# Performance work log

Measured on AMD Instinct MI355X. Metric: run time of the kernel, lower is better.

## Reference

```python
import jax, jax.numpy as jnp
import numpy as np

N_USER, N_ITEM, N_ENT, N_REL, D = 100000, 50000, 200000, 32, 64
N_EDGE, NNZ = 500000, 2000000
N_HOPS, N_GCN, RES_LAMBDA = 2, 2, 0.5
MIN_NORM = 1e-15
BALL_EPS = 1e-3  # Poincare ball (c=1) boundary clip, standard fp32 value


def _sqnorm(x):
    return jnp.sum(x * x, axis=-1, keepdims=True)


def _norm(x):
    return jnp.maximum(jnp.sqrt(_sqnorm(x)), MIN_NORM)


def project(x):
    # clip points to the open unit ball
    n = _norm(x)
    maxn = 1.0 - BALL_EPS
    return jnp.where(n > maxn, x / n * maxn, x)


def expmap0(u):
    # exp map at origin, c=1: tanh(||u||) * u/||u||
    n = _norm(u)
    return jnp.tanh(n) * u / n


def mobius_add(x, y):
    x2, y2 = _sqnorm(x), _sqnorm(y)
    xy = jnp.sum(x * y, axis=-1, keepdims=True)
    num = (1.0 + 2.0 * xy + y2) * x + (1.0 - x2) * y
    den = 1.0 + 2.0 * xy + x2 * y2
    return num / jnp.maximum(den, MIN_NORM)


def expmap(u, p):
    # exp map at base point p of tangent vector u
    n = _norm(u)
    lam = 2.0 / jnp.maximum(1.0 - _sqnorm(p), MIN_NORM)
    return mobius_add(p, jnp.tanh(0.5 * lam * n) * u / n)


def logmap(x, p):
    # log map at base point p of point x
    sub = mobius_add(-p, x)
    n = _norm(sub)
    lam = 2.0 / jnp.maximum(1.0 - _sqnorm(p), MIN_NORM)
    return (2.0 / lam) * jnp.arctanh(jnp.minimum(n, 1.0 - 1e-5)) * sub / n


def l2norm(x):
    # F.normalize(x, dim=-1), eps=1e-12
    return x / jnp.maximum(jnp.linalg.norm(x, axis=-1, keepdims=True), 1e-12)


def rgat_agg(ent, rel, head, tail, rtype):
    he, te, re = ent[head], ent[tail], rel[rtype]  # [E, D] gathers
    ricci = l2norm(te + re)
    hh = expmap0(he)
    ht = expmap(te, hh)
    hr = expmap(re, hh)
    res = project(mobius_add(ht, hr))
    res = logmap(res, hh) + ricci * 1e-7
    res = jax.nn.relu(res)
    sums = jax.ops.segment_sum(res, head, num_segments=N_ENT)
    cnt = jax.ops.segment_sum(jnp.ones((head.shape[0], 1), res.dtype), head, num_segments=N_ENT)
    return sums / jnp.maximum(cnt, 1.0)  # scatter_mean


def setup_inputs() -> dict:
    key = jax.random.key(0)
    ks = jax.random.split(key, 9)
    return {
        "uEmbeds": jax.random.normal(ks[0], (N_USER, D), jnp.float32) * 0.02,
        "eEmbeds": jax.random.normal(ks[1], (N_ENT, D), jnp.float32) * 0.02,
        "rEmbeds": jax.random.normal(ks[2], (N_REL, D), jnp.float32) * 0.02,
        "adj_val": jax.random.uniform(ks[8], (NNZ,), jnp.float32),
        "edge_head": jax.random.randint(ks[3], (N_EDGE,), 0, N_ENT),
        "edge_tail": jax.random.randint(ks[4], (N_EDGE,), 0, N_ENT),
        "edge_type": jax.random.randint(ks[5], (N_EDGE,), 1, N_REL),
        "adj_row": jax.random.randint(ks[6], (NNZ,), 0, N_USER + N_ITEM),
        "adj_col": jax.random.randint(ks[7], (NNZ,), 0, N_USER + N_ITEM),
    }


def reference(uEmbeds, eEmbeds, rEmbeds, adj_val, edge_head, edge_tail, edge_type, adj_row, adj_col):
    rtype = edge_type - 1
    ent_res = eEmbeds
    ent = eEmbeds
    for _ in range(N_HOPS):  # RGAT hops (mess_dropout=False for determinism)
        ent = rgat_agg(ent, rEmbeds, edge_head, edge_tail, rtype)
        ent = l2norm(ent)
        ent_res = RES_LAMBDA * ent_res + ent
    # concat users with first n_items entity embeddings
    embeds = jnp.concatenate([uEmbeds, ent_res[:N_ITEM]], axis=0)  # [user+item, D]
    total = embeds
    cur = embeds
    for _ in range(N_GCN):  # GCN layers: spmm(adj, embeds) in COO form
        cur = jax.ops.segment_sum(adj_val[:, None] * cur[adj_col], adj_row,
                                  num_segments=N_USER + N_ITEM)
        total = total + cur
    # original returns (total[:N_USER], total[N_USER:]); we return the concat
    return total
```

## Files before the change

kernel.cpp:

```cpp
#include <hip/hip_runtime.h>
#include <math.h>

#define D 64
#define MIN_NORM 1e-15f
#define NBINS 64
#define MAXBKT 1024
#define L1_TILE 4096

#define RCP(x)  __builtin_amdgcn_rcpf(x)
#define RSQ(x)  __builtin_amdgcn_rsqf(x)

template <int CTRL>
__device__ __forceinline__ float dpp_sum_step(float v) {
    int iv = __builtin_bit_cast(int, v);
    int sh = __builtin_amdgcn_update_dpp(0, iv, CTRL, 0xf, 0xf, true);
    return v + __builtin_bit_cast(float, sh);
}
#define DPP_XOR1  0xB1
#define DPP_XOR2  0x4E
#define DPP_HMIR  0x141
#define DPP_MIR   0x140

__device__ __forceinline__ float row16_sum(float v) {
    v = dpp_sum_step<DPP_XOR1>(v);
    v = dpp_sum_step<DPP_XOR2>(v);
    v = dpp_sum_step<DPP_HMIR>(v);
    v = dpp_sum_step<DPP_MIR>(v);
    return v;
}


__device__ __forceinline__ float fast_tanh_pos(float x) {
    float t = __expf(-2.0f * x);
    return (1.0f - t) * RCP(1.0f + t);
}

__device__ __forceinline__ float fast_atanh(float x) {
    return 0.5f * __logf((1.0f + x) * RCP(1.0f - x));
}


__global__ void rel_prep_kernel(const float* __restrict__ rel,
                                float* __restrict__ rtab, int n_rel)
{
    int r = threadIdx.x;
    if (r >= n_rel) return;
    float s = 0.0f;
    for (int d = 0; d < D; ++d) { float v = rel[r * D + d]; s += v * v; }
    float re2g = fmaxf(s, 1e-30f);
    float rn  = RSQ(re2g);
    float nre = re2g * rn;
    float a   = fast_tanh_pos(1.0f);
    float rm2 = RCP(fmaxf(1.0f - a * a, MIN_NORM));
    rtab[r]       = s;
    rtab[64 + r]  = rn;
    rtab[128 + r] = nre;
    rtab[192 + r] = fast_tanh_pos(nre * rm2) * rn;
}


template <int HOP>
__global__ __launch_bounds__(256) void rgat_head_kernel(
    const float* __restrict__ ent, const float* __restrict__ rel,
    const int* __restrict__ erow_ptr, const int2* __restrict__ pair_e,
    const int* __restrict__ headperm,
    const float* __restrict__ prev_res,
    const float* __restrict__ rtab, float* __restrict__ te2tab,
    float* __restrict__ ent_out, float* __restrict__ res_out,
    int n_ent)
{
    int g = blockIdx.x * 16 + (threadIdx.x >> 4);
    if (g >= n_ent) return;
    int sub = threadIdx.x & 15;
    int h = headperm[g];

    const float* hp = ent + (size_t)h * D + sub;
    float hex = hp[0], hey = hp[16], hez = hp[32], hew = hp[48];

    float HE2, a, HH2, mterm, rmterm, bconst;
    if (HOP == 1) {
        HE2 = row16_sum(hex*hex + hey*hey + hez*hez + hew*hew);
        float HE2g = fmaxf(HE2, 1e-30f);
        float rNhe = RSQ(HE2g);
        float Nhe  = HE2g * rNhe;
        a = fast_tanh_pos(Nhe) * rNhe;
        HH2 = a * a * HE2;
        mterm = fmaxf(1.0f - HH2, MIN_NORM);
        rmterm = RCP(mterm);
        bconst = 0.0f;
    } else {
        HE2 = 1.0f;
        a = fast_tanh_pos(1.0f);
        HH2 = a * a;
        mterm = 1.0f - HH2;
        rmterm = RCP(mterm);
        bconst = fast_tanh_pos(rmterm);
    }

    float ax = 0.0f, ay = 0.0f, az = 0.0f, aw = 0.0f;
    int s = erow_ptr[h];
    int e = erow_ptr[h + 1];

    for (int i = s; i < e; ++i) {
        int2 pe = pair_e[i];
        int tcol = pe.x;
        int rr = pe.y - 1;
        const float* tp = ent + (size_t)tcol * D + sub;
        const float* rp = rel + (size_t)rr * D + sub;
        float tex = tp[0], tey = tp[16], tez = tp[32], tew = tp[48];
        float rex = rp[0], rey = rp[16], rez = rp[32], rew = rp[48];

        float HT = row16_sum(hex*tex + hey*tey + hez*tez + hew*tew);
        float HR = row16_sum(hex*rex + hey*rey + hez*rez + hew*rew);
        float TR = row16_sum(tex*rex + tey*rey + tez*rez + tew*rew);

        float TE2;
        if (HOP == 1) TE2 = row16_sum(tex*tex + tey*tey + tez*tez + tew*tew);
        else          TE2 = te2tab[tcol];

        float RE2  = rtab[rr];
        float rNre = rtab[64 + rr];

        float ricci_k = 1e-7f * RSQ(fmaxf(TE2 + 2.0f * TR + RE2, 1e-24f));

        float b, c;
        if (HOP == 1) {
            float TE2g = fmaxf(TE2, 1e-30f);
            float rNte = RSQ(TE2g);
            b = fast_tanh_pos(TE2g * rNte * rmterm) * rNte;
            c = fast_tanh_pos(rtab[128 + rr] * rmterm) * rNre;
        } else {
            b = bconst;
            c = rtab[192 + rr];
        }

        float y2t = b * b * TE2, xyt = a * b * HT;
        float A1 = 1.0f + 2.0f * xyt + y2t, B1 = 1.0f - HH2;
        float r_d1 = RCP(fmaxf(1.0f + 2.0f * xyt + HH2 * y2t, MIN_NORM));
        float p1 = A1 * a * r_d1, q1 = B1 * b * r_d1;
        float HT2 = fmaxf((A1*A1*HH2 + 2.0f*A1*B1*xyt + B1*B1*y2t) * r_d1 * r_d1, 0.0f);

        float y2r = c * c * RE2, xyr = a * c * HR;
        float A2 = 1.0f + 2.0f * xyr + y2r, B2 = 1.0f - HH2;
        float r_d2 = RCP(fmaxf(1.0f + 2.0f * xyr + HH2 * y2r, MIN_NORM));
        float p2 = A2 * a * r_d2, q2 = B2 * c * r_d2;
        float HR2 = fmaxf((A2*A2*HH2 + 2.0f*A2*B2*xyr + B2*B2*y2r) * r_d2 * r_d2, 0.0f);

        float xy3 = p1*p2*HE2 + p1*q2*HR + q1*p2*HT + q1*q2*TR;
        float A3 = 1.0f + 2.0f * xy3 + HR2, B3 = 1.0f - HT2;
        float r_d3 = RCP(fmaxf(1.0f + 2.0f * xy3 + HT2 * HR2, MIN_NORM));
        float al = (A3 * p1 + B3 * p2) * r_d3;
        float be = A3 * q1 * r_d3;
        float ga = B3 * q2 * r_d3;
        float R2 = fmaxf((A3*A3*HT2 + 2.0f*A3*B3*xy3 + B3*B3*HR2) * r_d3 * r_d3, 0.0f);

        float R2g = fmaxf(R2, 1e-30f);
        float rNr = RSQ(R2g);
        float Nr  = R2g * rNr;
        const float maxn = 1.0f - 1e-3f;
        if (Nr > maxn) {
            float sc = maxn * rNr;
            al *= sc; be *= sc; ga *= sc;
            R2 = maxn * maxn;
        }

        float dhr = a * (al * HE2 + be * HT + ga * HR);
        float xy4 = -dhr;
        float A4 = 1.0f + 2.0f * xy4 + R2, B4 = 1.0f - HH2;
        float r_d4 = RCP(fmaxf(1.0f + 2.0f * xy4 + HH2 * R2, MIN_NORM));
        float sh = (-A4 * a + B4 * al) * r_d4;
        float st = B4 * be * r_d4;
        float sr = B4 * ga * r_d4;
        float SUB2 = fmaxf((A4*A4*HH2 + 2.0f*A4*B4*xy4 + B4*B4*R2) * r_d4 * r_d4, 0.0f);

        float SUB2g = fmaxf(SUB2, 1e-30f);
        float rNsub = RSQ(SUB2g);
        float Nsub  = SUB2g * rNsub;
        float k = mterm * fast_atanh(fminf(Nsub, 1.0f - 1e-5f)) * rNsub;

        float kh = k * sh;
        float kt = k * st + ricci_k;
        float kr = k * sr + ricci_k;

        ax += fmaxf(kh*hex + kt*tex + kr*rex, 0.0f);
        ay += fmaxf(kh*hey + kt*tey + kr*rey, 0.0f);
        az += fmaxf(kh*hez + kt*tez + kr*rez, 0.0f);
        aw += fmaxf(kh*hew + kt*tew + kr*rew, 0.0f);
    }

    float rc = RCP(fmaxf((float)(e - s), 1.0f));
    float mx = ax*rc, my = ay*rc, mz = az*rc, mw = aw*rc;
    float M2 = row16_sum(mx*mx + my*my + mz*mz + mw*mw);
    float rn = RSQ(fmaxf(M2, 1e-24f));
    mx *= rn; my *= rn; mz *= rn; mw *= rn;

    if (HOP == 1) {
        float* ep = ent_out + (size_t)h * D + sub;
        ep[0] = mx; ep[16] = my; ep[32] = mz; ep[48] = mw;
        if (sub == 0) te2tab[h] = (M2 > 1e-24f) ? 1.0f : 0.0f;
    }
    const float* pp = prev_res + (size_t)h * D + sub;
    float* rp2 = res_out + (size_t)h * D + sub;
    rp2[0]  = 0.5f*pp[0]  + mx;
    rp2[16] = 0.5f*pp[16] + my;
    rp2[32] = 0.5f*pp[32] + mz;
    rp2[48] = 0.5f*pp[48] + mw;
}


__global__ __launch_bounds__(256) void deg_hist_kernel(
    const int* __restrict__ erow_ptr, int* __restrict__ dbins, int n_heads)
{
    __shared__ int lbin[NBINS];
    int tid = threadIdx.x;
    if (tid < NBINS) lbin[tid] = 0;
    __syncthreads();
    int h = blockIdx.x * 256 + tid;
    if (h < n_heads) {
        int d = min(erow_ptr[h + 1] - erow_ptr[h], NBINS - 1);
        atomicAdd(&lbin[d], 1);
    }
    __syncthreads();
    if (tid < NBINS) { int c = lbin[tid]; if (c) atomicAdd(&dbins[tid], c); }
}

__global__ void deg_scan_kernel(const int* __restrict__ dbins, int* __restrict__ bin_cursor)
{
    int tid = threadIdx.x;
    int v = dbins[tid];
    int incl = v;
#pragma unroll
    for (int off = 1; off < 64; off <<= 1) {
        int u = __shfl_up(incl, off, 64);
        if (tid >= off) incl += u;
    }
    int T = __shfl(incl, 63, 64);
    bin_cursor[tid] = T - incl;
}

__global__ __launch_bounds__(256) void deg_scatter_kernel(
    const int* __restrict__ erow_ptr, int* __restrict__ bin_cursor,
    int* __restrict__ headperm, int n_heads)
{
    __shared__ int lbin[NBINS];
    __shared__ int lbase[NBINS];
    int tid = threadIdx.x;
    if (tid < NBINS) lbin[tid] = 0;
    __syncthreads();
    int h = blockIdx.x * 256 + tid;
    int b = 0, lpos = 0;
    bool act = (h < n_heads);
    if (act) {
        b = min(erow_ptr[h + 1] - erow_ptr[h], NBINS - 1);
        lpos = atomicAdd(&lbin[b], 1);
    }
    __syncthreads();
    if (tid < NBINS) { int c = lbin[tid]; lbase[tid] = c ? atomicAdd(&bin_cursor[tid], c) : 0; }
    __syncthreads();
    if (act) headperm[lbase[b] + lpos] = h;
}


__global__ void concat_init_kernel(const float4* __restrict__ u,
                                   const float4* __restrict__ res,
                                   float4* __restrict__ bufA,
                                   int user4, int total4)
{
    int i = blockIdx.x * blockDim.x + threadIdx.x;
    if (i >= total4) return;
    float4 v = (i < user4) ? u[i] : res[i - user4];
    bufA[i] = v;
}


__global__ void hist_kernel(const int* __restrict__ row, int* __restrict__ counts, int nnz)
{
    int i = blockIdx.x * blockDim.x + threadIdx.x;
    if (i < nnz) atomicAdd(&counts[row[i]], 1);
}

__global__ __launch_bounds__(256) void block_scan_kernel(
    const int* __restrict__ counts, int* __restrict__ local_scan,
    int* __restrict__ block_sums, int n)
{
    __shared__ int wsum[4];
    int tid  = threadIdx.x;
    int lane = tid & 63;
    int wave = tid >> 6;
    int base = blockIdx.x * 1024 + tid * 4;

    int4 v = make_int4(0, 0, 0, 0);
    if (base + 3 < n) {
        v = *(const int4*)(counts + base);
    } else {
        if (base + 0 < n) v.x = counts[base + 0];
        if (base + 1 < n) v.y = counts[base + 1];
        if (base + 2 < n) v.z = counts[base + 2];
        if (base + 3 < n) v.w = counts[base + 3];
    }
    int total = v.x + v.y + v.z + v.w;

    int incl = total;
#pragma unroll
    for (int off = 1; off < 64; off <<= 1) {
        int u = __shfl_up(incl, off, 64);
        if (lane >= off) incl += u;
    }
    if (lane == 63) wsum[wave] = incl;
    __syncthreads();
    int woff = 0;
    for (int w = 0; w < wave; ++w) woff += wsum[w];
    int excl = woff + incl - total;

    if (tid == 255) block_sums[blockIdx.x] = woff + incl;

    int p0 = excl;
    int p1 = p0 + v.x;
    int p2 = p1 + v.y;
    int p3 = p2 + v.z;
    if (base + 3 < n) {
        *(int4*)(local_scan + base) = make_int4(p0, p1, p2, p3);
    } else {
        if (base + 0 < n) local_scan[base + 0] = p0;
        if (base + 1 < n) local_scan[base + 1] = p1;
        if (base + 2 < n) local_scan[base + 2] = p2;
        if (base + 3 < n) local_scan[base + 3] = p3;
    }
}

__global__ __launch_bounds__(256) void scan_blocksums_kernel(
    const int* __restrict__ block_sums, int* __restrict__ block_offs,
    int* __restrict__ row_ptr, int n, int nb)
{
    __shared__ int lds[256];
    int tid = threadIdx.x;
    int v = (tid < nb) ? block_sums[tid] : 0;
    lds[tid] = v;
    __syncthreads();
    for (int off = 1; off < 256; off <<= 1) {
        int t = (tid >= off) ? lds[tid - off] : 0;
        __syncthreads();
        lds[tid] += t;
        __syncthreads();
    }
    block_offs[tid] = lds[tid] - v;
    if (tid == nb - 1) row_ptr[n] = lds[tid];
}

__global__ void apply_offsets_kernel(const int* __restrict__ local_scan,
                                     const int* __restrict__ block_offs,
                                     int* __restrict__ row_ptr,
                                     int* __restrict__ cursor,
                                     int* __restrict__ bktcur, int n)
{
    int i = blockIdx.x * blockDim.x + threadIdx.x;
    if (i >= n) return;
    int v = local_scan[i] + block_offs[i >> 10];
    row_ptr[i] = v;
    cursor[i]  = v;
    if ((i & 255) == 0) bktcur[i >> 8] = v;
}


__global__ __launch_bounds__(256) void bucket_l1_kernel(
    const int* __restrict__ key, const int* __restrict__ col,
    const int* __restrict__ vbits,
    int* __restrict__ bktcur, int2* __restrict__ bkt,
    int n, int nbkt)
{
    __shared__ int lcnt[MAXBKT];
    __shared__ int lofs[MAXBKT];
    __shared__ int gofs[MAXBKT];
    __shared__ int lpos[MAXBKT];
    __shared__ int wsum[4];
    __shared__ int2 lent[L1_TILE];
    __shared__ unsigned short lbkt[L1_TILE];

    int tid  = threadIdx.x;
    int lane = tid & 63;
    int wave = tid >> 6;
    int base = blockIdx.x * L1_TILE;
    int cnt_total = min(n - base, L1_TILE);

    for (int b = tid; b < MAXBKT; b += 256) lcnt[b] = 0;
    __syncthreads();

#pragma unroll
    for (int k = 0; k < L1_TILE / 256; ++k) {
        int i = base + k * 256 + tid;
        if (i < n) atomicAdd(&lcnt[key[i] >> 8], 1);
    }
    __syncthreads();

    int b0 = tid * 4;
    int c0 = lcnt[b0], c1 = lcnt[b0 + 1], c2 = lcnt[b0 + 2], c3 = lcnt[b0 + 3];
    int tot = c0 + c1 + c2 + c3;
    int incl = tot;
#pragma unroll
    for (int off = 1; off < 64; off <<= 1) {
        int u = __shfl_up(incl, off, 64);
        if (lane >= off) incl += u;
    }
    if (lane == 63) wsum[wave] = incl;
    __syncthreads();
    int woff = 0;
    for (int w = 0; w < wave; ++w) woff += wsum[w];
    int excl = woff + incl - tot;
    lofs[b0]     = excl;                lpos[b0]     = excl;
    lofs[b0 + 1] = excl + c0;           lpos[b0 + 1] = excl + c0;
    lofs[b0 + 2] = excl + c0 + c1;      lpos[b0 + 2] = excl + c0 + c1;
    lofs[b0 + 3] = excl + c0 + c1 + c2; lpos[b0 + 3] = excl + c0 + c1 + c2;
    for (int b = tid; b < nbkt; b += 256) {
        int c = lcnt[b];
        gofs[b] = c ? atomicAdd(&bktcur[b], c) : 0;
    }
    __syncthreads();

#pragma unroll
    for (int k = 0; k < L1_TILE / 256; ++k) {
        int i = base + k * 256 + tid;
        if (i < n) {
            int r = key[i];
            int b = r >> 8;
            int p = atomicAdd(&lpos[b], 1);
            lent[p] = make_int2((col[i] << 8) | (r & 255), vbits[i]);
            lbkt[p] = (unsigned short)b;
        }
    }
    __syncthreads();

    for (int j = tid; j < cnt_total; j += 256) {
        int b = lbkt[j];
        bkt[gofs[b] + (j - lofs[b])] = lent[j];
    }
}

__global__ __launch_bounds__(256) void place_l2_kernel(
    const int* __restrict__ row_ptr, const int2* __restrict__ bkt,
    int* __restrict__ cursor, int2* __restrict__ pair, int nkeys)
{
    int b = blockIdx.x;
    int rbase = b << 8;
    int s = row_ptr[min(rbase, nkeys)];
    int e = row_ptr[min(rbase + 256, nkeys)];
    for (int i = s + (int)threadIdx.x; i < e; i += 256) {
        int2 q = bkt[i];
        int pos = atomicAdd(&cursor[rbase + (q.x & 255)], 1);
        pair[pos] = make_int2(q.x >> 8, q.y);
    }
}


__device__ __forceinline__ float spmm_row_gather(
    const int2* __restrict__ pair, const float* __restrict__ cur,
    int s, int e, int lane)
{
    int cnt = e - s;
    if (cnt <= 0) return 0.0f;
    int nv = min(cnt, 64);
    int2 q = pair[s + min(lane, nv - 1)];

    float acc0 = 0.0f, acc1 = 0.0f, acc2 = 0.0f, acc3 = 0.0f;
    float acc4 = 0.0f, acc5 = 0.0f, acc6 = 0.0f, acc7 = 0.0f;

    for (int base = 0; base < nv; base += 8) {
        int c0 = __builtin_amdgcn_readlane(q.x, base + 0);
        int c1 = __builtin_amdgcn_readlane(q.x, base + 1);
        int c2 = __builtin_amdgcn_readlane(q.x, base + 2);
        int c3 = __builtin_amdgcn_readlane(q.x, base + 3);
        int c4 = __builtin_amdgcn_readlane(q.x, base + 4);
        int c5 = __builtin_amdgcn_readlane(q.x, base + 5);
        int c6 = __builtin_amdgcn_readlane(q.x, base + 6);
        int c7 = __builtin_amdgcn_readlane(q.x, base + 7);
        float x0 = cur[(size_t)c0 * D + lane];
        float x1 = cur[(size_t)c1 * D + lane];
        float x2 = cur[(size_t)c2 * D + lane];
        float x3 = cur[(size_t)c3 * D + lane];
        float x4 = cur[(size_t)c4 * D + lane];
        float x5 = cur[(size_t)c5 * D + lane];
        float x6 = cur[(size_t)c6 * D + lane];
        float x7 = cur[(size_t)c7 * D + lane];
        float v0 = (base + 0 < nv) ? __int_as_float(__builtin_amdgcn_readlane(q.y, base + 0)) : 0.0f;
        float v1 = (base + 1 < nv) ? __int_as_float(__builtin_amdgcn_readlane(q.y, base + 1)) : 0.0f;
        float v2 = (base + 2 < nv) ? __int_as_float(__builtin_amdgcn_readlane(q.y, base + 2)) : 0.0f;
        float v3 = (base + 3 < nv) ? __int_as_float(__builtin_amdgcn_readlane(q.y, base + 3)) : 0.0f;
        float v4 = (base + 4 < nv) ? __int_as_float(__builtin_amdgcn_readlane(q.y, base + 4)) : 0.0f;
        float v5 = (base + 5 < nv) ? __int_as_float(__builtin_amdgcn_readlane(q.y, base + 5)) : 0.0f;
        float v6 = (base + 6 < nv) ? __int_as_float(__builtin_amdgcn_readlane(q.y, base + 6)) : 0.0f;
        float v7 = (base + 7 < nv) ? __int_as_float(__builtin_amdgcn_readlane(q.y, base + 7)) : 0.0f;
        acc0 = fmaf(v0, x0, acc0);
        acc1 = fmaf(v1, x1, acc1);
        acc2 = fmaf(v2, x2, acc2);
        acc3 = fmaf(v3, x3, acc3);
        acc4 = fmaf(v4, x4, acc4);
        acc5 = fmaf(v5, x5, acc5);
        acc6 = fmaf(v6, x6, acc6);
        acc7 = fmaf(v7, x7, acc7);
    }
    for (int i = s + 64; i < e; ++i) {
        int2 p = pair[i];
        acc0 = fmaf(__int_as_float(p.y), cur[(size_t)p.x * D + lane], acc0);
    }
    return ((acc0 + acc1) + (acc2 + acc3)) + ((acc4 + acc5) + (acc6 + acc7));
}

__global__ __launch_bounds__(256) void spmm_l1_kernel(
    const int* __restrict__ row_ptr, const int2* __restrict__ pair,
    const float* __restrict__ cur, float* __restrict__ nxt, int n_rows)
{
    int row = blockIdx.x * 4 + (threadIdx.x >> 6);
    if (row >= n_rows) return;
    int lane = threadIdx.x & 63;
    int s = row_ptr[row];
    int e = row_ptr[row + 1];
    float acc = spmm_row_gather(pair, cur, s, e, lane);
    nxt[(size_t)row * D + lane] = acc;
}

__global__ __launch_bounds__(256) void spmm_l2_kernel(
    const int* __restrict__ row_ptr, const int2* __restrict__ pair,
    const float* __restrict__ cur1, const float* __restrict__ embeds,
    float* __restrict__ out, int n_rows)
{
    int row = blockIdx.x * 4 + (threadIdx.x >> 6);
    if (row >= n_rows) return;
    int lane = threadIdx.x & 63;
    int s = row_ptr[row];
    int e = row_ptr[row + 1];
    float acc = spmm_row_gather(pair, cur1, s, e, lane);
    size_t idx = (size_t)row * D + lane;
    float emb = __builtin_nontemporal_load(embeds + idx);
    float c1  = cur1[idx];
    __builtin_nontemporal_store(emb + c1 + acc, out + idx);
}


extern "C" void kernel_launch(void* const* d_in, const int* in_sizes, int n_in,
                              void* d_out, int out_size, void* d_ws, size_t ws_size,
                              hipStream_t stream)
{
    const float* uE      = (const float*)d_in[0];
    const float* eE      = (const float*)d_in[1];
    const float* rE      = (const float*)d_in[2];
    const float* adj_val = (const float*)d_in[3];
    const int*   e_head  = (const int*)d_in[4];
    const int*   e_tail  = (const int*)d_in[5];
    const int*   e_type  = (const int*)d_in[6];
    const int*   a_row   = (const int*)d_in[7];
    const int*   a_col   = (const int*)d_in[8];

    const int n_user  = in_sizes[0] / D;
    const int n_ent   = in_sizes[1] / D;
    const int n_rel   = in_sizes[2] / D;
    const int nnz     = in_sizes[3];
    const int n_edges = in_sizes[4];
    const int n_rows  = out_size / D;

    float* ws = (float*)d_ws;
    const size_t entElems = (size_t)n_ent * D;
    float* ent1    = ws;
    float* ent_res = ws + entElems;
    int*   r3      = (int*)(ws + 2 * entElems);

    int2* ebkt = (int2*)ent_res;
    int2* abkt = (int2*)ent_res;

    const int nep = n_ent + 4;
    int*  erow_ptr = r3;
    int*  ecursor  = erow_ptr + nep;
    int2* pair_e   = (int2*)(ecursor + nep);
    int*  headperm = (int*)(pair_e + n_edges);
    int*  elocal   = headperm + n_ent;
    int*  ebsums   = elocal + n_ent;
    int*  eboffs   = ebsums + 256;
    int*  dbins    = eboffs + 256;
    int*  bincur   = dbins + NBINS;
    int*  ebktcur  = bincur + NBINS;
    float* te2tab  = (float*)(ebktcur + MAXBKT);
    float* rtab    = te2tab + n_ent;

    int*  row_ptr    = r3;
    int*  cursor     = row_ptr + (n_rows + 4);
    int2* pair       = (int2*)(cursor + n_rows + 4);
    int*  local_scan = (int*)(pair + nnz);
    int*  block_sums = local_scan + n_rows;
    int*  block_offs = block_sums + 256;
    int*  abktcur    = block_offs + 256;

    float* out = (float*)d_out;

    const int enb    = (n_ent + 1023) / 1024;
    const int nbkt_e = (n_ent + 255) / 256;
    hipMemsetAsync(ecursor, 0, (size_t)nep * sizeof(int), stream);
    hipMemsetAsync(dbins, 0, 2 * NBINS * sizeof(int), stream);
    rel_prep_kernel<<<1, 64, 0, stream>>>(rE, rtab, n_rel);
    hist_kernel<<<(n_edges + 255) / 256, 256, 0, stream>>>(e_head, ecursor, n_edges);
    block_scan_kernel<<<enb, 256, 0, stream>>>(ecursor, elocal, ebsums, n_ent);
    scan_blocksums_kernel<<<1, 256, 0, stream>>>(ebsums, eboffs, erow_ptr, n_ent, enb);
    apply_offsets_kernel<<<(n_ent + 255) / 256, 256, 0, stream>>>(elocal, eboffs,
                                                                  erow_ptr, ecursor,
                                                                  ebktcur, n_ent);
    bucket_l1_kernel<<<(n_edges + L1_TILE - 1) / L1_TILE, 256, 0, stream>>>(
        e_head, e_tail, (const int*)e_type, ebktcur, ebkt, n_edges, nbkt_e);
    place_l2_kernel<<<nbkt_e, 256, 0, stream>>>(erow_ptr, ebkt, ecursor, pair_e, n_ent);
    deg_hist_kernel<<<(n_ent + 255) / 256, 256, 0, stream>>>(erow_ptr, dbins, n_ent);
    deg_scan_kernel<<<1, 64, 0, stream>>>(dbins, bincur);
    deg_scatter_kernel<<<(n_ent + 255) / 256, 256, 0, stream>>>(erow_ptr, bincur,
                                                                headperm, n_ent);

    const int head_blocks = (n_ent + 15) / 16;
    rgat_head_kernel<1><<<head_blocks, 256, 0, stream>>>(eE, rE, erow_ptr, pair_e,
                                                         headperm, eE, rtab, te2tab,
                                                         ent1, ent_res, n_ent);
    rgat_head_kernel<2><<<head_blocks, 256, 0, stream>>>(ent1, rE, erow_ptr, pair_e,
                                                         headperm, ent_res, rtab, te2tab,
                                                         ent1, ent_res, n_ent);

    float* bufA = ent1;
    float* bufB = ent_res;

    const int total4 = n_rows * (D / 4);
    const int user4  = n_user * (D / 4);

    concat_init_kernel<<<(total4 + 255) / 256, 256, 0, stream>>>(
        (const float4*)uE, (const float4*)ent_res, (float4*)bufA, user4, total4);

    const int nb     = (n_rows + 1023) / 1024;
    const int nbkt_a = (n_rows + 255) / 256;
    hipMemsetAsync(cursor, 0, (size_t)(n_rows + 1) * sizeof(int), stream);
    hist_kernel<<<(nnz + 255) / 256, 256, 0, stream>>>(a_row, cursor, nnz);
    block_scan_kernel<<<nb, 256, 0, stream>>>(cursor, local_scan, block_sums, n_rows);
    scan_blocksums_kernel<<<1, 256, 0, stream>>>(block_sums, block_offs, row_ptr, n_rows, nb);
    apply_offsets_kernel<<<(n_rows + 255) / 256, 256, 0, stream>>>(local_scan, block_offs,
                                                                   row_ptr, cursor,
                                                                   abktcur, n_rows);
    bucket_l1_kernel<<<(nnz + L1_TILE - 1) / L1_TILE, 256, 0, stream>>>(
        a_row, a_col, (const int*)adj_val, abktcur, abkt, nnz, nbkt_a);
    place_l2_kernel<<<nbkt_a, 256, 0, stream>>>(row_ptr, abkt, cursor, pair, n_rows);

    const int row_blocks = (n_rows + 3) / 4;
    spmm_l1_kernel<<<row_blocks, 256, 0, stream>>>(row_ptr, pair, bufA, bufB, n_rows);
    spmm_l2_kernel<<<row_blocks, 256, 0, stream>>>(row_ptr, pair, bufB, bufA, out, n_rows);
}
```

Before: 691.5 us.

## Replace histogram+scan CSR build with fixed-capacity window buckets and per-window placement

```diff
diff --git a/kernel.cpp b/kernel.cpp
--- a/kernel.cpp
+++ b/kernel.cpp
@@ -6,6 +6,8 @@
 #define NBINS 64
 #define MAXBKT 1024
 #define L1_TILE 4096
+#define WCAP_A 3840
+#define WCAP_E 1024
 
 #define RCP(x)  __builtin_amdgcn_rcpf(x)
 #define RSQ(x)  __builtin_amdgcn_rsqf(x)
@@ -273,100 +275,11 @@
 }
 
 
-__global__ void hist_kernel(const int* __restrict__ row, int* __restrict__ counts, int nnz)
-{
-    int i = blockIdx.x * blockDim.x + threadIdx.x;
-    if (i < nnz) atomicAdd(&counts[row[i]], 1);
-}
-
-__global__ __launch_bounds__(256) void block_scan_kernel(
-    const int* __restrict__ counts, int* __restrict__ local_scan,
-    int* __restrict__ block_sums, int n)
-{
-    __shared__ int wsum[4];
-    int tid  = threadIdx.x;
-    int lane = tid & 63;
-    int wave = tid >> 6;
-    int base = blockIdx.x * 1024 + tid * 4;
-
-    int4 v = make_int4(0, 0, 0, 0);
-    if (base + 3 < n) {
-        v = *(const int4*)(counts + base);
-    } else {
-        if (base + 0 < n) v.x = counts[base + 0];
-        if (base + 1 < n) v.y = counts[base + 1];
-        if (base + 2 < n) v.z = counts[base + 2];
-        if (base + 3 < n) v.w = counts[base + 3];
-    }
-    int total = v.x + v.y + v.z + v.w;
-
-    int incl = total;
-#pragma unroll
-    for (int off = 1; off < 64; off <<= 1) {
-        int u = __shfl_up(incl, off, 64);
-        if (lane >= off) incl += u;
-    }
-    if (lane == 63) wsum[wave] = incl;
-    __syncthreads();
-    int woff = 0;
-    for (int w = 0; w < wave; ++w) woff += wsum[w];
-    int excl = woff + incl - total;
-
-    if (tid == 255) block_sums[blockIdx.x] = woff + incl;
-
-    int p0 = excl;
-    int p1 = p0 + v.x;
-    int p2 = p1 + v.y;
-    int p3 = p2 + v.z;
-    if (base + 3 < n) {
-        *(int4*)(local_scan + base) = make_int4(p0, p1, p2, p3);
-    } else {
-        if (base + 0 < n) local_scan[base + 0] = p0;
-        if (base + 1 < n) local_scan[base + 1] = p1;
-        if (base + 2 < n) local_scan[base + 2] = p2;
-        if (base + 3 < n) local_scan[base + 3] = p3;
-    }
-}
-
-__global__ __launch_bounds__(256) void scan_blocksums_kernel(
-    const int* __restrict__ block_sums, int* __restrict__ block_offs,
-    int* __restrict__ row_ptr, int n, int nb)
-{
-    __shared__ int lds[256];
-    int tid = threadIdx.x;
-    int v = (tid < nb) ? block_sums[tid] : 0;
-    lds[tid] = v;
-    __syncthreads();
-    for (int off = 1; off < 256; off <<= 1) {
-        int t = (tid >= off) ? lds[tid - off] : 0;
-        __syncthreads();
-        lds[tid] += t;
-        __syncthreads();
-    }
-    block_offs[tid] = lds[tid] - v;
-    if (tid == nb - 1) row_ptr[n] = lds[tid];
-}
-
-__global__ void apply_offsets_kernel(const int* __restrict__ local_scan,
-                                     const int* __restrict__ block_offs,
-                                     int* __restrict__ row_ptr,
-                                     int* __restrict__ cursor,
-                                     int* __restrict__ bktcur, int n)
-{
-    int i = blockIdx.x * blockDim.x + threadIdx.x;
-    if (i >= n) return;
-    int v = local_scan[i] + block_offs[i >> 10];
-    row_ptr[i] = v;
-    cursor[i]  = v;
-    if ((i & 255) == 0) bktcur[i >> 8] = v;
-}
-
-
 __global__ __launch_bounds__(256) void bucket_l1_kernel(
     const int* __restrict__ key, const int* __restrict__ col,
     const int* __restrict__ vbits,
     int* __restrict__ bktcur, int2* __restrict__ bkt,
-    int n, int nbkt)
+    int n, int nbkt, int cap)
 {
     __shared__ int lcnt[MAXBKT];
     __shared__ int lofs[MAXBKT];
@@ -431,21 +344,83 @@
 
     for (int j = tid; j < cnt_total; j += 256) {
         int b = lbkt[j];
-        bkt[gofs[b] + (j - lofs[b])] = lent[j];
-    }
-}
-
-__global__ __launch_bounds__(256) void place_l2_kernel(
-    const int* __restrict__ row_ptr, const int2* __restrict__ bkt,
-    int* __restrict__ cursor, int2* __restrict__ pair, int nkeys)
-{
-    int b = blockIdx.x;
-    int rbase = b << 8;
-    int s = row_ptr[min(rbase, nkeys)];
-    int e = row_ptr[min(rbase + 256, nkeys)];
-    for (int i = s + (int)threadIdx.x; i < e; i += 256) {
-        int2 q = bkt[i];
-        int pos = atomicAdd(&cursor[rbase + (q.x & 255)], 1);
+        int off = gofs[b] + (j - lofs[b]);
+        if (off < cap) bkt[(size_t)b * cap + off] = lent[j];
+    }
+}
+
+__global__ __launch_bounds__(256) void win_scan_kernel(
+    const int* __restrict__ wincnt, int* __restrict__ winbase, int nwin, int cap)
+{
+    __shared__ int wsum[4];
+    int tid = threadIdx.x, lane = tid & 63, wave = tid >> 6;
+    int b = tid * 4;
+    int c0 = (b + 0 < nwin) ? min(wincnt[b + 0], cap) : 0;
+    int c1 = (b + 1 < nwin) ? min(wincnt[b + 1], cap) : 0;
+    int c2 = (b + 2 < nwin) ? min(wincnt[b + 2], cap) : 0;
+    int c3 = (b + 3 < nwin) ? min(wincnt[b + 3], cap) : 0;
+    int tot = c0 + c1 + c2 + c3;
+    int incl = tot;
+#pragma unroll
+    for (int off = 1; off < 64; off <<= 1) {
+        int u = __shfl_up(incl, off, 64);
+        if (lane >= off) incl += u;
+    }
+    if (lane == 63) wsum[wave] = incl;
+    __syncthreads();
+    int woff = 0;
+    for (int w = 0; w < wave; ++w) woff += wsum[w];
+    int excl = woff + incl - tot;
+    if (b + 0 < nwin) winbase[b + 0] = excl;
+    if (b + 1 < nwin) winbase[b + 1] = excl + c0;
+    if (b + 2 < nwin) winbase[b + 2] = excl + c0 + c1;
+    if (b + 3 < nwin) winbase[b + 3] = excl + c0 + c1 + c2;
+}
+
+__global__ __launch_bounds__(256) void place_l2b_kernel(
+    const int* __restrict__ wincnt, const int* __restrict__ winbase,
+    const int2* __restrict__ bkt,
+    int2* __restrict__ pair, int* __restrict__ row_ptr,
+    int n_keys, int nwin, int cap)
+{
+    __shared__ int rcnt[256];
+    __shared__ int rofs[256];
+    __shared__ int wsum[4];
+    int w = blockIdx.x;
+    int tid = threadIdx.x;
+    int lane = tid & 63, wave = tid >> 6;
+    int rbase = w << 8;
+    int cnt = min(wincnt[w], cap);
+    int base = winbase[w];
+    const int2* seg = bkt + (size_t)w * cap;
+
+    rcnt[tid] = 0;
+    __syncthreads();
+    for (int i = tid; i < cnt; i += 256)
+        atomicAdd(&rcnt[bkt[(size_t)w * cap + i].x & 255], 1);
+    __syncthreads();
+
+    int v = rcnt[tid];
+    int incl = v;
+#pragma unroll
+    for (int off = 1; off < 64; off <<= 1) {
+        int u = __shfl_up(incl, off, 64);
+        if (lane >= off) incl += u;
+    }
+    if (lane == 63) wsum[wave] = incl;
+    __syncthreads();
+    int woff = 0;
+    for (int i = 0; i < wave; ++i) woff += wsum[i];
+    int excl = woff + incl - v;
+    rofs[tid] = excl;
+    int r = rbase + tid;
+    if (r < n_keys) row_ptr[r] = base + excl;
+    if (w == nwin - 1 && tid == 255) row_ptr[n_keys] = base + excl + v;
+    __syncthreads();
+
+    for (int i = tid; i < cnt; i += 256) {
+        int2 q = seg[i];
+        int pos = base + atomicAdd(&rofs[q.x & 255], 1);
         pair[pos] = make_int2(q.x >> 8, q.y);
     }
 }
@@ -567,42 +542,30 @@
 
     const int nep = n_ent + 4;
     int*  erow_ptr = r3;
-    int*  ecursor  = erow_ptr + nep;
-    int2* pair_e   = (int2*)(ecursor + nep);
+    int2* pair_e   = (int2*)(erow_ptr + nep);
     int*  headperm = (int*)(pair_e + n_edges);
-    int*  elocal   = headperm + n_ent;
-    int*  ebsums   = elocal + n_ent;
-    int*  eboffs   = ebsums + 256;
-    int*  dbins    = eboffs + 256;
+    int*  dbins    = headperm + n_ent;
     int*  bincur   = dbins + NBINS;
-    int*  ebktcur  = bincur + NBINS;
-    float* te2tab  = (float*)(ebktcur + MAXBKT);
+    int*  ewincur  = bincur + NBINS;
+    int*  ewinbase = ewincur + MAXBKT;
+    float* te2tab  = (float*)(ewinbase + MAXBKT);
     float* rtab    = te2tab + n_ent;
 
-    int*  row_ptr    = r3;
-    int*  cursor     = row_ptr + (n_rows + 4);
-    int2* pair       = (int2*)(cursor + n_rows + 4);
-    int*  local_scan = (int*)(pair + nnz);
-    int*  block_sums = local_scan + n_rows;
-    int*  block_offs = block_sums + 256;
-    int*  abktcur    = block_offs + 256;
+    int*  row_ptr  = r3;
+    int2* pair     = (int2*)(row_ptr + (n_rows + 4));
+    int*  awincur  = (int*)(pair + nnz);
+    int*  awinbase = awincur + MAXBKT;
 
     float* out = (float*)d_out;
 
-    const int enb    = (n_ent + 1023) / 1024;
     const int nbkt_e = (n_ent + 255) / 256;
-    hipMemsetAsync(ecursor, 0, (size_t)nep * sizeof(int), stream);
-    hipMemsetAsync(dbins, 0, 2 * NBINS * sizeof(int), stream);
+    hipMemsetAsync(dbins, 0, (2 * NBINS + MAXBKT) * sizeof(int), stream);
     rel_prep_kernel<<<1, 64, 0, stream>>>(rE, rtab, n_rel);
-    hist_kernel<<<(n_edges + 255) / 256, 256, 0, stream>>>(e_head, ecursor, n_edges);
-    block_scan_kernel<<<enb, 256, 0, stream>>>(ecursor, elocal, ebsums, n_ent);
-    scan_blocksums_kernel<<<1, 256, 0, stream>>>(ebsums, eboffs, erow_ptr, n_ent, enb);
-    apply_offsets_kernel<<<(n_ent + 255) / 256, 256, 0, stream>>>(elocal, eboffs,
-                                                                  erow_ptr, ecursor,
-                                                                  ebktcur, n_ent);
     bucket_l1_kernel<<<(n_edges + L1_TILE - 1) / L1_TILE, 256, 0, stream>>>(
-        e_head, e_tail, (const int*)e_type, ebktcur, ebkt, n_edges, nbkt_e);
-    place_l2_kernel<<<nbkt_e, 256, 0, stream>>>(erow_ptr, ebkt, ecursor, pair_e, n_ent);
+        e_head, e_tail, (const int*)e_type, ewincur, ebkt, n_edges, nbkt_e, WCAP_E);
+    win_scan_kernel<<<1, 256, 0, stream>>>(ewincur, ewinbase, nbkt_e, WCAP_E);
+    place_l2b_kernel<<<nbkt_e, 256, 0, stream>>>(ewincur, ewinbase, ebkt,
+                                                 pair_e, erow_ptr, n_ent, nbkt_e, WCAP_E);
     deg_hist_kernel<<<(n_ent + 255) / 256, 256, 0, stream>>>(erow_ptr, dbins, n_ent);
     deg_scan_kernel<<<1, 64, 0, stream>>>(dbins, bincur);
     deg_scatter_kernel<<<(n_ent + 255) / 256, 256, 0, stream>>>(erow_ptr, bincur,
@@ -625,18 +588,13 @@
     concat_init_kernel<<<(total4 + 255) / 256, 256, 0, stream>>>(
         (const float4*)uE, (const float4*)ent_res, (float4*)bufA, user4, total4);
 
-    const int nb     = (n_rows + 1023) / 1024;
     const int nbkt_a = (n_rows + 255) / 256;
-    hipMemsetAsync(cursor, 0, (size_t)(n_rows + 1) * sizeof(int), stream);
-    hist_kernel<<<(nnz + 255) / 256, 256, 0, stream>>>(a_row, cursor, nnz);
-    block_scan_kernel<<<nb, 256, 0, stream>>>(cursor, local_scan, block_sums, n_rows);
-    scan_blocksums_kernel<<<1, 256, 0, stream>>>(block_sums, block_offs, row_ptr, n_rows, nb);
-    apply_offsets_kernel<<<(n_rows + 255) / 256, 256, 0, stream>>>(local_scan, block_offs,
-                                                                   row_ptr, cursor,
-                                                                   abktcur, n_rows);
+    hipMemsetAsync(awincur, 0, (size_t)MAXBKT * sizeof(int), stream);
     bucket_l1_kernel<<<(nnz + L1_TILE - 1) / L1_TILE, 256, 0, stream>>>(
-        a_row, a_col, (const int*)adj_val, abktcur, abkt, nnz, nbkt_a);
-    place_l2_kernel<<<nbkt_a, 256, 0, stream>>>(row_ptr, abkt, cursor, pair, n_rows);
+        a_row, a_col, (const int*)adj_val, awincur, abkt, nnz, nbkt_a, WCAP_A);
+    win_scan_kernel<<<1, 256, 0, stream>>>(awincur, awinbase, nbkt_a, WCAP_A);
+    place_l2b_kernel<<<nbkt_a, 256, 0, stream>>>(awincur, awinbase, abkt,
+                                                 pair, row_ptr, n_rows, nbkt_a, WCAP_A);
 
     const int row_blocks = (n_rows + 3) / 4;
     spmm_l1_kernel<<<row_blocks, 256, 0, stream>>>(row_ptr, pair, bufA, bufB, n_rows);
```

After: 555.9 us. 19.6% less time.
